# Performance work log

Hardware: AMD Instinct MI355X
Metric: run time of the kernel (lower is better)

## Reference

```python
import jax, jax.numpy as jnp
import numpy as np

EPS = 1e-5

def layer_norm(x, w, b):
    mu = x.mean(-1, keepdims=True)
    var = x.var(-1, keepdims=True)
    return (x - mu) / jnp.sqrt(var + EPS) * w + b

def moe_ffn(y, gW, W1, b1, W2, b2, topk):
    # y: [B,N,d]; W1: [E,d,f]; W2: [E,f,d].  Dense-equivalent of the
    # torch gather/compute/scatter-add dispatch: every expert runs on every
    # token, combined with top-k gate weights (zero for unselected experts).
    gate = jax.nn.softmax(y @ gW, axis=-1)                       # [B,N,E]
    w, sel = jax.lax.top_k(gate, topk)                           # [B,N,k]
    onehot = jax.nn.one_hot(sel, gW.shape[-1], dtype=y.dtype)    # [B,N,k,E]
    comb = jnp.einsum('bnk,bnke->bne', w, onehot)                # combine weights
    hmid = jax.nn.gelu(jnp.einsum('bnd,edf->bnef', y, W1) + b1, approximate=False)
    eo = jnp.einsum('bnef,efd->bned', hmid, W2) + b2             # [B,N,E,d]
    out = jnp.einsum('bne,bned->bnd', comb, eo)
    mask = onehot.sum(2)                                         # [B,N,E] 0/1
    cnt = mask.sum((0, 1))                                       # tokens per expert
    emb = jnp.einsum('bne,bnd->ed', mask, y) / jnp.maximum(cnt, 1.0)[:, None]
    return out, gate, emb

def setup_inputs():
    B, S, N = 8, 512, 1024
    d, H, E, f, L, topk = 512, 8, 8, 8, 2, 2   # d_ff == n_heads (repo quirk)
    key = jax.random.key(0)
    ks = iter(jax.random.split(key, 40))
    g = lambda shape, s=0.02: jax.random.normal(next(ks), shape, jnp.float32) * s
    return dict(
        x=jax.random.normal(next(ks), (B, S, N), jnp.float32),
        revin_w=jnp.ones((N,), jnp.float32) + g((N,), 0.01),
        revin_b=g((N,), 0.01),
        emb_W=g((S, d)), emb_b=g((d,)),
        Wq=g((L, d, d)), bq=g((L, d)),
        Wk=g((L, d, d)), bk=g((L, d)),
        Wv=g((L, d, d)), bv=g((L, d)),
        Wo=g((L, d, d)), bo=g((L, d)),
        ln1_w=jnp.ones((L, d), jnp.float32), ln1_b=jnp.zeros((L, d), jnp.float32),
        ln2_w=jnp.ones((L, d), jnp.float32), ln2_b=jnp.zeros((L, d), jnp.float32),
        gate_W=g((L, d, E)),
        eW1=g((L, E, d, f)), eb1=g((L, E, f)),
        eW2=g((L, E, f, d)), eb2=g((L, E, d)),
        enc_norm_w=jnp.ones((d,), jnp.float32), enc_norm_b=jnp.zeros((d,), jnp.float32),
        head_gate_W=g((d, E)),
        head_W=g((E, d, d)), head_b=g((E, d)),
        topk=topk, n_heads=H,
    )

def reference(x, revin_w, revin_b, emb_W, emb_b, Wq, bq, Wk, bk, Wv, bv, Wo, bo,
              ln1_w, ln1_b, ln2_w, ln2_b, gate_W, eW1, eb1, eW2, eb2,
              enc_norm_w, enc_norm_b, head_gate_W, head_W, head_b, topk, n_heads):
    B, S, N = x.shape
    d = emb_W.shape[1]
    H = n_heads
    dh = d // H
    L = Wq.shape[0]
    # RevIN normalize over time per variable (dropout layers are eval/identity)
    xv = jnp.swapaxes(x, 1, 2)                                   # [B,N,S]
    mean = xv.mean(-1, keepdims=True)
    std = jnp.sqrt(xv.var(-1, keepdims=True) + EPS)
    xn = (xv - mean) / std * revin_w[None, :, None] + revin_b[None, :, None]
    # DataEmbedding_inverted: Linear over the time axis -> variable tokens
    h = xn @ emb_W + emb_b                                       # [B,N,d]
    for l in range(L):
        q = (h @ Wq[l] + bq[l]).reshape(B, N, H, dh)
        k = (h @ Wk[l] + bk[l]).reshape(B, N, H, dh)
        v = (h @ Wv[l] + bv[l]).reshape(B, N, H, dh)
        attn = jax.nn.softmax(jnp.einsum('bnhe,bmhe->bhnm', q, k) / jnp.sqrt(jnp.float32(dh)), axis=-1)
        o = jnp.einsum('bhnm,bmhe->bnhe', attn, v).reshape(B, N, d) @ Wo[l] + bo[l]
        h = layer_norm(h + o, ln1_w[l], ln1_b[l])
        ffn, _gate, _emb = moe_ffn(h, gate_W[l], eW1[l], eb1[l], eW2[l], eb2[l], topk)
        h = layer_norm(h + ffn, ln2_w[l], ln2_b[l])
    h = layer_norm(h, enc_norm_w, enc_norm_b)
    # MoE projection head: experts are Linear(d, d)
    gate = jax.nn.softmax(h @ head_gate_W, axis=-1)
    w, sel = jax.lax.top_k(gate, topk)
    onehot = jax.nn.one_hot(sel, head_gate_W.shape[-1], dtype=h.dtype)
    comb = jnp.einsum('bnk,bnke->bne', w, onehot)
    eo = jnp.einsum('bnd,edf->bnef', h, head_W) + head_b         # [B,N,E,d]
    out = jnp.einsum('bne,bned->bnd', comb, eo)                  # [B,N,d]
    # RevIN denorm applied on [B, d_model, N]
    o2 = jnp.swapaxes(out, 1, 2)
    o2 = (o2 - revin_b[None, None, :]) / (revin_w[None, None, :] + 1e-10)
    o2 = o2 * jnp.swapaxes(std, 1, 2) + jnp.swapaxes(mean, 1, 2)
    return jnp.swapaxes(o2, 1, 2)                                # [B, n_vars, d_model]
```

## Files before the change

kernel.cpp:

```cpp
#include <hip/hip_runtime.h>
#include <math.h>

#define BATCH 8
#define SEQ 512
#define NVAR 1024
#define DM 512
#define NH 8
#define DH 64
#define NE 8
#define NF 8
#define NL 2
#define NTOK (BATCH*NVAR)
#define LN_EPS 1e-5f
#define LSC 2048.0f
#define ILSC (1.0f/2048.0f)

typedef __attribute__((ext_vector_type(8))) _Float16 f16x8;
typedef __attribute__((ext_vector_type(4))) float f32x4;
#define MFMA16 __builtin_amdgcn_mfma_f32_16x16x32_f16

__device__ __forceinline__ void fsplit(float v, _Float16& hi, _Float16& lo) {
    hi = (_Float16)v;
    lo = (_Float16)((v - (float)hi) * LSC);
}
__device__ __forceinline__ float frec(_Float16 hi, _Float16 lo) {
    return (float)hi + (float)lo * ILSC;
}

__device__ __forceinline__ void gload_lds16(const _Float16* g, _Float16* l) {
    __builtin_amdgcn_global_load_lds(
        (const __attribute__((address_space(1))) void*)g,
        (__attribute__((address_space(3))) void*)l, 16, 0, 0);
}

#define DPPROR(v, C) __int_as_float(__builtin_amdgcn_update_dpp(0, __float_as_int(v), (C), 0xF, 0xF, true))
__device__ __forceinline__ float rowmax16(float v) {
    v = fmaxf(v, DPPROR(v, 0x121));
    v = fmaxf(v, DPPROR(v, 0x122));
    v = fmaxf(v, DPPROR(v, 0x124));
    v = fmaxf(v, DPPROR(v, 0x128));
    return v;
}
__device__ __forceinline__ float rowsum16(float v) {
    v += DPPROR(v, 0x121);
    v += DPPROR(v, 0x122);
    v += DPPROR(v, 0x124);
    v += DPPROR(v, 0x128);
    return v;
}

__global__ __launch_bounds__(256) void revin_stats_kernel(
        const float* __restrict__ x, float* __restrict__ mean, float* __restrict__ stdd) {
    int blk = blockIdx.x;
    int b = blk >> 4;
    int n0 = (blk & 15) << 6;
    int t = threadIdx.x;
    int ni = t & 63, sg = t >> 6;
    float s = 0.f, ss = 0.f;
    for (int sidx = sg; sidx < SEQ; sidx += 4) {
        float v = x[((size_t)b*SEQ + sidx)*NVAR + n0 + ni];
        s += v; ss += v*v;
    }
    __shared__ float rs[4][64], rq[4][64];
    rs[sg][ni] = s; rq[sg][ni] = ss;
    __syncthreads();
    if (t < 64) {
        float su = rs[0][t] + rs[1][t] + rs[2][t] + rs[3][t];
        float sq = rq[0][t] + rq[1][t] + rq[2][t] + rq[3][t];
        float m  = su / (float)SEQ;
        float var = sq / (float)SEQ - m*m;
        int n = n0 + t;
        mean[b*NVAR + n] = m;
        stdd[b*NVAR + n] = sqrtf(var + LN_EPS);
    }
}

__global__ __launch_bounds__(256) void revin_norm_kernel(
        const float* __restrict__ x, const float* __restrict__ mean, const float* __restrict__ stdd,
        const float* __restrict__ rw, const float* __restrict__ rb,
        _Float16* __restrict__ xnhi, _Float16* __restrict__ xnlo) {
    __shared__ float tile[32][33];
    int n0 = blockIdx.x << 5, s0 = blockIdx.y << 5, b = blockIdx.z;
    int t = threadIdx.x;
    int j = t & 31, i0 = t >> 5;
    for (int ii = i0; ii < 32; ii += 8)
        tile[ii][j] = x[((size_t)b*SEQ + s0 + ii)*NVAR + n0 + j];
    __syncthreads();
    int si = t & 31, j0 = t >> 5;
    for (int nj = j0; nj < 32; nj += 8) {
        int n = n0 + nj;
        float m = mean[b*NVAR + n], sd = stdd[b*NVAR + n];
        float v = (tile[si][nj] - m) / sd * rw[n] + rb[n];
        _Float16 h_, l_; fsplit(v, h_, l_);
        size_t idx = ((size_t)b*NVAR + n)*SEQ + s0 + si;
        xnhi[idx] = h_; xnlo[idx] = l_;
    }
}

struct WSrcs { const float* p[9]; };
__global__ __launch_bounds__(256) void transpose_w_kernel(
        WSrcs srcs, _Float16* __restrict__ whi, _Float16* __restrict__ wlo) {
    const float* W = srcs.p[blockIdx.z];
    _Float16* oh = whi + (size_t)blockIdx.z * DM * DM;
    _Float16* ol = wlo + (size_t)blockIdx.z * DM * DM;
    __shared__ float tile[64][65];
    int k0 = blockIdx.x << 6, n0 = blockIdx.y << 6;
    int t = threadIdx.x;
    for (int idx = t; idx < 4096; idx += 256) {
        int k = idx >> 6, n = idx & 63;
        tile[k][n] = W[(size_t)(k0 + k)*DM + n0 + n];
    }
    __syncthreads();
    for (int idx = t; idx < 4096; idx += 256) {
        int n = idx >> 6, k = idx & 63;
        _Float16 h_, l_; fsplit(tile[k][n], h_, l_);
        size_t o = (size_t)(n0 + n)*DM + k0 + k;
        oh[o] = h_; ol[o] = l_;
    }
}

__global__ __launch_bounds__(256) void gemm_f16x2_kernel(
        const _Float16* __restrict__ Ahg, const _Float16* __restrict__ Alg,
        const _Float16* __restrict__ Whg, const _Float16* __restrict__ Wlg,
        const float* __restrict__ bias, float* __restrict__ C,
        _Float16* __restrict__ Chi, _Float16* __restrict__ Clo,
        int M, int K, int N) {
    __shared__ _Float16 smem[24576];
    int id = blockIdx.x + (blockIdx.y << 3);
    int rm = ((id & 7) << 6) | (id >> 3);
    int bm = (rm >> 3) << 7, bn = (rm & 7) << 6;
    int t = threadIdx.x;
    int w = t >> 6, lane = t & 63, m16 = lane & 15, quad = lane >> 4;
    int wv = __builtin_amdgcn_readfirstlane(w);
    int lrow = lane >> 2, lcol = (lane & 3) << 3;
    f32x4 a1[2][4] = {}, a2[2][4] = {};

    #define G_STAGE(c, kk) do {                                              \
        _Pragma("unroll")                                                    \
        for (int ch = 0; ch < 2; ++ch) {                                     \
            size_t ga = (size_t)(bm + wv*32 + ch*16 + lrow)*K + (kk) + lcol; \
            gload_lds16(&Ahg[ga], &smem[(c)*4096 + (wv*32 + ch*16)*32]);     \
            gload_lds16(&Alg[ga], &smem[8192 + (c)*4096 + (wv*32 + ch*16)*32]); \
        }                                                                    \
        size_t gb = (size_t)(bn + wv*16 + lrow)*K + (kk) + lcol;             \
        gload_lds16(&Whg[gb], &smem[16384 + (c)*2048 + (wv*16)*32]);         \
        gload_lds16(&Wlg[gb], &smem[20480 + (c)*2048 + (wv*16)*32]);         \
    } while (0)

    G_STAGE(0, 0);
    int cur = 0;
    for (int k0 = 0; k0 < K; k0 += 32, cur ^= 1) {
        __syncthreads();
        if (k0 + 32 < K) G_STAGE(cur ^ 1, k0 + 32);
        const _Float16* AH = &smem[cur*4096];
        const _Float16* AL = &smem[8192 + cur*4096];
        const _Float16* BH = &smem[16384 + cur*2048];
        const _Float16* BL = &smem[20480 + cur*2048];
        f16x8 bh_[4], bl_[4];
#pragma unroll
        for (int nt = 0; nt < 4; ++nt) {
            bh_[nt] = *(const f16x8*)&BH[(nt*16 + m16)*32 + quad*8];
            bl_[nt] = *(const f16x8*)&BL[(nt*16 + m16)*32 + quad*8];
        }
#pragma unroll
        for (int h2 = 0; h2 < 2; ++h2) {
            f16x8 ah = *(const f16x8*)&AH[(w*32 + h2*16 + m16)*32 + quad*8];
            f16x8 al = *(const f16x8*)&AL[(w*32 + h2*16 + m16)*32 + quad*8];
#pragma unroll
            for (int nt = 0; nt < 4; ++nt) {
                a1[h2][nt] = MFMA16(ah, bh_[nt], a1[h2][nt], 0, 0, 0);
                a2[h2][nt] = MFMA16(ah, bl_[nt], a2[h2][nt], 0, 0, 0);
                a2[h2][nt] = MFMA16(al, bh_[nt], a2[h2][nt], 0, 0, 0);
            }
        }
    }
    #undef G_STAGE
#pragma unroll
    for (int h2 = 0; h2 < 2; ++h2)
#pragma unroll
        for (int nt = 0; nt < 4; ++nt) {
            int col = bn + nt*16 + m16;
            float bv = bias[col];
#pragma unroll
            for (int r = 0; r < 4; ++r) {
                size_t row = bm + w*32 + h2*16 + quad*4 + r;
                float v = a1[h2][nt][r] + a2[h2][nt][r]*ILSC + bv;
                if (C) C[row*N + col] = v;
                if (Chi) {
                    _Float16 h_, l_; fsplit(v, h_, l_);
                    Chi[row*N + col] = h_; Clo[row*N + col] = l_;
                }
            }
        }
}

__global__ __launch_bounds__(256) void gemm_f16x2_vt_kernel(
        const _Float16* __restrict__ Ahg, const _Float16* __restrict__ Alg,
        const _Float16* __restrict__ Whg, const _Float16* __restrict__ Wlg,
        const float* __restrict__ bias,
        _Float16* __restrict__ vthi, _Float16* __restrict__ vtlo) {
    __shared__ _Float16 smem[24576];
    int id = blockIdx.x + (blockIdx.y << 3);
    int rm = ((id & 7) << 6) | (id >> 3);
    int bm = (rm >> 3) << 7, bn = (rm & 7) << 6;
    int t = threadIdx.x;
    int w = t >> 6, lane = t & 63, m16 = lane & 15, quad = lane >> 4;
    int wv = __builtin_amdgcn_readfirstlane(w);
    int lrow = lane >> 2, lcol = (lane & 3) << 3;
    f32x4 a1[2][4] = {}, a2[2][4] = {};

    #define G_STAGE(c, kk) do {                                              \
        _Pragma("unroll")                                                    \
        for (int ch = 0; ch < 2; ++ch) {                                     \
            size_t ga = (size_t)(bm + wv*32 + ch*16 + lrow)*DM + (kk) + lcol;\
            gload_lds16(&Ahg[ga], &smem[(c)*4096 + (wv*32 + ch*16)*32]);     \
            gload_lds16(&Alg[ga], &smem[8192 + (c)*4096 + (wv*32 + ch*16)*32]); \
        }                                                                    \
        size_t gb = (size_t)(bn + wv*16 + lrow)*DM + (kk) + lcol;            \
        gload_lds16(&Whg[gb], &smem[16384 + (c)*2048 + (wv*16)*32]);         \
        gload_lds16(&Wlg[gb], &smem[20480 + (c)*2048 + (wv*16)*32]);         \
    } while (0)

    G_STAGE(0, 0);
    int cur = 0;
    for (int k0 = 0; k0 < DM; k0 += 32, cur ^= 1) {
        __syncthreads();
        if (k0 + 32 < DM) G_STAGE(cur ^ 1, k0 + 32);
        const _Float16* AH = &smem[cur*4096];
        const _Float16* AL = &smem[8192 + cur*4096];
        const _Float16* BH = &smem[16384 + cur*2048];
        const _Float16* BL = &smem[20480 + cur*2048];
        f16x8 bh_[4], bl_[4];
#pragma unroll
        for (int nt = 0; nt < 4; ++nt) {
            bh_[nt] = *(const f16x8*)&BH[(nt*16 + m16)*32 + quad*8];
            bl_[nt] = *(const f16x8*)&BL[(nt*16 + m16)*32 + quad*8];
        }
#pragma unroll
        for (int h2 = 0; h2 < 2; ++h2) {
            f16x8 ah = *(const f16x8*)&AH[(w*32 + h2*16 + m16)*32 + quad*8];
            f16x8 al = *(const f16x8*)&AL[(w*32 + h2*16 + m16)*32 + quad*8];
#pragma unroll
            for (int nt = 0; nt < 4; ++nt) {
                a1[h2][nt] = MFMA16(ah, bh_[nt], a1[h2][nt], 0, 0, 0);
                a2[h2][nt] = MFMA16(ah, bl_[nt], a2[h2][nt], 0, 0, 0);
                a2[h2][nt] = MFMA16(al, bh_[nt], a2[h2][nt], 0, 0, 0);
            }
        }
    }
    #undef G_STAGE
    __syncthreads();
    float (*Ct)[65] = (float (*)[65])smem;
#pragma unroll
    for (int h2 = 0; h2 < 2; ++h2)
#pragma unroll
        for (int nt = 0; nt < 4; ++nt) {
            float bv = bias[bn + nt*16 + m16];
#pragma unroll
            for (int r = 0; r < 4; ++r)
                Ct[w*32 + h2*16 + quad*4 + r][nt*16 + m16] = a1[h2][nt][r] + a2[h2][nt][r]*ILSC + bv;
        }
    __syncthreads();
    int b = bm >> 10, tokn0 = bm & 1023, hh = bn >> 6;
    int dh = t >> 2, tg = (t & 3) << 4;
    size_t rowb = ((size_t)(b*8 + hh)*64 + dh)*NVAR + tokn0;
    for (int hb = 0; hb < 2; ++hb) {
        int tl0 = hb*64 + tg;
        unsigned short hbuf[16], lbuf[16];
#pragma unroll
        for (int i = 0; i < 16; ++i) {
            _Float16 h_, l_; fsplit(Ct[tl0 + i][dh], h_, l_);
            hbuf[i] = __builtin_bit_cast(unsigned short, h_);
            lbuf[i] = __builtin_bit_cast(unsigned short, l_);
        }
        uint4 uh0, uh1, ul0, ul1;
        uh0.x = hbuf[0]|(hbuf[1]<<16);  uh0.y = hbuf[2]|(hbuf[3]<<16);
        uh0.z = hbuf[4]|(hbuf[5]<<16);  uh0.w = hbuf[6]|(hbuf[7]<<16);
        uh1.x = hbuf[8]|(hbuf[9]<<16);  uh1.y = hbuf[10]|(hbuf[11]<<16);
        uh1.z = hbuf[12]|(hbuf[13]<<16);uh1.w = hbuf[14]|(hbuf[15]<<16);
        ul0.x = lbuf[0]|(lbuf[1]<<16);  ul0.y = lbuf[2]|(lbuf[3]<<16);
        ul0.z = lbuf[4]|(lbuf[5]<<16);  ul0.w = lbuf[6]|(lbuf[7]<<16);
        ul1.x = lbuf[8]|(lbuf[9]<<16);  ul1.y = lbuf[10]|(lbuf[11]<<16);
        ul1.z = lbuf[12]|(lbuf[13]<<16);ul1.w = lbuf[14]|(lbuf[15]<<16);
        *(uint4*)&vthi[rowb + tl0]     = uh0;
        *(uint4*)&vthi[rowb + tl0 + 8] = uh1;
        *(uint4*)&vtlo[rowb + tl0]     = ul0;
        *(uint4*)&vtlo[rowb + tl0 + 8] = ul1;
    }
}

__global__ __launch_bounds__(256, 4) void attn_f16x2_kernel(
        const _Float16* __restrict__ qh, const _Float16* __restrict__ ql,
        const _Float16* __restrict__ kh, const _Float16* __restrict__ kl,
        const _Float16* __restrict__ vth, const _Float16* __restrict__ vtl,
        _Float16* __restrict__ oh, _Float16* __restrict__ ol) {
    __shared__ _Float16 Kh[64][72], Kl[64][72];
    __shared__ _Float16 Vh[64][72], Vl[64][72];
    int blk = blockIdx.x;
    blk = ((blk & 7) << 7) | (blk >> 3);
    int qt = blk & 15, bh = blk >> 4;
    int b = bh >> 3, hh = bh & 7;
    int q0 = qt << 6;
    int t = threadIdx.x;
    int w = t >> 6, lane = t & 63;
    int m16 = lane & 15, quad = lane >> 4;
    size_t bbase = (size_t)b * NVAR;
    size_t vbase = (size_t)bh * DH * NVAR;

    f16x8 qfh[2], qfl[2];
#pragma unroll
    for (int ks = 0; ks < 2; ++ks) {
        size_t gq = (bbase + q0 + w*16 + m16)*DM + hh*DH + ks*32 + quad*8;
        qfh[ks] = *(const f16x8*)&qh[gq] * (_Float16)0.125f;
        qfl[ks] = *(const f16x8*)&ql[gq] * (_Float16)0.125f;
    }

    float mrow[4] = {-1e30f,-1e30f,-1e30f,-1e30f};
    float lrow[4] = {0.f,0.f,0.f,0.f};
    f32x4 o1[4] = {}, o2[4] = {};

    for (int n0 = 0; n0 < NVAR; n0 += 64) {
        for (int idx = t; idx < 512; idx += 256) {
            int r = idx >> 3, cg = (idx & 7) << 3;
            size_t gk = (bbase + n0 + r)*DM + hh*DH + cg;
            size_t gv = vbase + (size_t)r*NVAR + n0 + cg;
            *(uint4*)&Kh[r][cg] = *(const uint4*)&kh[gk];
            *(uint4*)&Kl[r][cg] = *(const uint4*)&kl[gk];
            *(uint4*)&Vh[r][cg] = *(const uint4*)&vth[gv];
            *(uint4*)&Vl[r][cg] = *(const uint4*)&vtl[gv];
        }
        __syncthreads();

        f32x4 s1[4] = {}, s2[4] = {};
#pragma unroll
        for (int ks = 0; ks < 2; ++ks) {
#pragma unroll
            for (int nt = 0; nt < 4; ++nt) {
                f16x8 bh_ = *(const f16x8*)&Kh[nt*16 + m16][ks*32 + quad*8];
                f16x8 bl_ = *(const f16x8*)&Kl[nt*16 + m16][ks*32 + quad*8];
                s1[nt] = MFMA16(qfh[ks], bh_, s1[nt], 0, 0, 0);
                s2[nt] = MFMA16(qfh[ks], bl_, s2[nt], 0, 0, 0);
                s2[nt] = MFMA16(qfl[ks], bh_, s2[nt], 0, 0, 0);
            }
        }
        __syncthreads();

        float pbuf[4][4];
        float mx[4];
#pragma unroll
        for (int r = 0; r < 4; ++r) {
            float sv0 = fmaf(s2[0][r], ILSC, s1[0][r]);
            float sv1 = fmaf(s2[1][r], ILSC, s1[1][r]);
            float sv2 = fmaf(s2[2][r], ILSC, s1[2][r]);
            float sv3 = fmaf(s2[3][r], ILSC, s1[3][r]);
            pbuf[0][r] = sv0; pbuf[1][r] = sv1; pbuf[2][r] = sv2; pbuf[3][r] = sv3;
            mx[r] = rowmax16(fmaxf(fmaxf(sv0, sv1), fmaxf(sv2, sv3)));
        }
        bool grow = (mx[0] > mrow[0]) | (mx[1] > mrow[1]) |
                    (mx[2] > mrow[2]) | (mx[3] > mrow[3]);
        if (__any(grow)) {
#pragma unroll
            for (int r = 0; r < 4; ++r) {
                float mnew = fmaxf(mrow[r], mx[r]);
                float alpha = __expf(mrow[r] - mnew);
                mrow[r] = mnew;
                lrow[r] *= alpha;
#pragma unroll
                for (int nt = 0; nt < 4; ++nt) { o1[nt][r] *= alpha; o2[nt][r] *= alpha; }
            }
        }
#pragma unroll
        for (int r = 0; r < 4; ++r) {
            float p0 = __expf(pbuf[0][r] - mrow[r]);
            float p1 = __expf(pbuf[1][r] - mrow[r]);
            float p2 = __expf(pbuf[2][r] - mrow[r]);
            float p3 = __expf(pbuf[3][r] - mrow[r]);
            lrow[r] += rowsum16(p0 + p1 + p2 + p3);
            pbuf[0][r] = p0; pbuf[1][r] = p1; pbuf[2][r] = p2; pbuf[3][r] = p3;
        }
#pragma unroll
        for (int nt = 0; nt < 4; ++nt)
#pragma unroll
            for (int r = 0; r < 4; ++r) {
                _Float16 h_, l_; fsplit(pbuf[nt][r], h_, l_);
                Kh[w*16 + quad*4 + r][nt*16 + m16] = h_;
                Kl[w*16 + quad*4 + r][nt*16 + m16] = l_;
            }

#pragma unroll
        for (int ks = 0; ks < 2; ++ks) {
            f16x8 ph = *(const f16x8*)&Kh[w*16 + m16][ks*32 + quad*8];
            f16x8 pl = *(const f16x8*)&Kl[w*16 + m16][ks*32 + quad*8];
#pragma unroll
            for (int nt = 0; nt < 4; ++nt) {
                f16x8 vh_ = *(const f16x8*)&Vh[nt*16 + m16][ks*32 + quad*8];
                f16x8 vl_ = *(const f16x8*)&Vl[nt*16 + m16][ks*32 + quad*8];
                o1[nt] = MFMA16(ph, vh_, o1[nt], 0, 0, 0);
                o2[nt] = MFMA16(ph, vl_, o2[nt], 0, 0, 0);
                o2[nt] = MFMA16(pl, vh_, o2[nt], 0, 0, 0);
            }
        }
        __syncthreads();
    }
#pragma unroll
    for (int r = 0; r < 4; ++r) {
        float inv = 1.0f / lrow[r];
        size_t rowp = (bbase + q0 + w*16 + quad*4 + r)*DM + hh*DH;
#pragma unroll
        for (int nt = 0; nt < 4; ++nt) {
            float ov = fmaf(o2[nt][r], ILSC, o1[nt][r]) * inv;
            _Float16 h_, l_; fsplit(ov, h_, l_);
            oh[rowp + nt*16 + m16] = h_;
            ol[rowp + nt*16 + m16] = l_;
        }
    }
}

__global__ __launch_bounds__(256) void ln_kernel(
        _Float16* __restrict__ hhi, _Float16* __restrict__ hlo,
        const float* __restrict__ res,
        const float* __restrict__ w, const float* __restrict__ b) {
    int rowi = blockIdx.x, t = threadIdx.x;
    size_t base = (size_t)rowi * DM;
    int c = t << 1;
    unsigned int uh = *(const unsigned int*)&hhi[base + c];
    unsigned int ul = *(const unsigned int*)&hlo[base + c];
    _Float16 h0 = __builtin_bit_cast(_Float16, (unsigned short)(uh & 0xFFFF));
    _Float16 h1 = __builtin_bit_cast(_Float16, (unsigned short)(uh >> 16));
    _Float16 l0 = __builtin_bit_cast(_Float16, (unsigned short)(ul & 0xFFFF));
    _Float16 l1 = __builtin_bit_cast(_Float16, (unsigned short)(ul >> 16));
    float v0 = frec(h0, l0);
    float v1 = frec(h1, l1);
    if (res) { float2 rv = *(const float2*)&res[base + c]; v0 += rv.x; v1 += rv.y; }
    float s = v0 + v1, q = v0*v0 + v1*v1;
#pragma unroll
    for (int off = 1; off < 64; off <<= 1) {
        s += __shfl_xor(s, off);
        q += __shfl_xor(q, off);
    }
    __shared__ float sred[4], qred[4];
    int wid = t >> 6, lane = t & 63;
    if (lane == 0) { sred[wid] = s; qred[wid] = q; }
    __syncthreads();
    s = sred[0] + sred[1] + sred[2] + sred[3];
    q = qred[0] + qred[1] + qred[2] + qred[3];
    float m = s / (float)DM;
    float var = q / (float)DM - m*m;
    float inv = 1.0f / sqrtf(var + LN_EPS);
    float2 wv = *(const float2*)&w[c];
    float2 bv = *(const float2*)&b[c];
    float y0 = (v0 - m)*inv * wv.x + bv.x;
    float y1 = (v1 - m)*inv * wv.y + bv.y;
    _Float16 h0o, l0o, h1o, l1o;
    fsplit(y0, h0o, l0o); fsplit(y1, h1o, l1o);
    *(unsigned int*)&hhi[base + c] =
        (unsigned int)__builtin_bit_cast(unsigned short, h0o) |
        ((unsigned int)__builtin_bit_cast(unsigned short, h1o) << 16);
    *(unsigned int*)&hlo[base + c] =
        (unsigned int)__builtin_bit_cast(unsigned short, l0o) |
        ((unsigned int)__builtin_bit_cast(unsigned short, l1o) << 16);
}

__device__ __forceinline__ float gelu_exact(float xv) {
    return 0.5f * xv * (1.0f + erff(xv * 0.70710678118654752f));
}

__global__ __launch_bounds__(256) void moe_kernel(
        const _Float16* __restrict__ hhi, const _Float16* __restrict__ hlo,
        float* __restrict__ out,
        const float* __restrict__ gW, const float* __restrict__ W1, const float* __restrict__ b1,
        const float* __restrict__ W2, const float* __restrict__ b2) {
    int tok = blockIdx.x, t = threadIdx.x;
    __shared__ float hs[DM];
    __shared__ float red[32][8];
    __shared__ float glog[8];
    __shared__ float hmid[8];
    __shared__ float wsel[2];
    __shared__ int   esel[2];
    size_t base = (size_t)tok * DM;
    hs[t] = frec(hhi[base + t], hlo[base + t]);
    hs[t + 256] = frec(hhi[base + t + 256], hlo[base + t + 256]);
    __syncthreads();
    int e = t & 7, i0 = t >> 3;
    {
        float a = 0.f;
        for (int i = i0; i < DM; i += 32) a += hs[i] * gW[i*NE + e];
        red[i0][e] = a;
    }
    __syncthreads();
    if (t < 8) { float sv = 0.f; for (int i = 0; i < 32; ++i) sv += red[i][t]; glog[t] = sv; }
    __syncthreads();
    if (t == 0) {
        float m0 = -1e30f, m1 = -1e30f; int s0i = 0, s1i = 0;
        for (int ei = 0; ei < 8; ++ei) {
            float vv = glog[ei];
            if (vv > m0) { m1 = m0; s1i = s0i; m0 = vv; s0i = ei; }
            else if (vv > m1) { m1 = vv; s1i = ei; }
        }
        float Z = 0.f;
        for (int ei = 0; ei < 8; ++ei) Z += expf(glog[ei] - m0);
        wsel[0] = 1.0f / Z;
        wsel[1] = expf(m1 - m0) / Z;
        esel[0] = s0i; esel[1] = s1i;
    }
    __syncthreads();
    float o0 = 0.f, o1 = 0.f;
    for (int ks = 0; ks < 2; ++ks) {
        int ee = esel[ks]; float wk = wsel[ks];
        int f = t & 7;
        float a = 0.f;
        for (int i = i0; i < DM; i += 32) a += hs[i] * W1[((size_t)ee*DM + i)*NF + f];
        red[i0][f] = a;
        __syncthreads();
        if (t < 8) {
            float sv = b1[ee*NF + t];
            for (int i = 0; i < 32; ++i) sv += red[i][t];
            hmid[t] = gelu_exact(sv);
        }
        __syncthreads();
        float s0v = b2[ee*DM + t], s1v = b2[ee*DM + t + 256];
#pragma unroll
        for (int i = 0; i < NF; ++i) {
            float hm = hmid[i];
            const float* wp = W2 + ((size_t)ee*NF + i)*DM;
            s0v += hm * wp[t]; s1v += hm * wp[t + 256];
        }
        o0 += wk * s0v; o1 += wk * s1v;
        __syncthreads();
    }
    out[base + t] = o0; out[base + t + 256] = o1;
}

__global__ __launch_bounds__(64) void head_init_kernel(int* __restrict__ cnt) {
    if (threadIdx.x < NE) cnt[threadIdx.x] = 0;
}

__global__ __launch_bounds__(256) void head_gate_kernel(
        const _Float16* __restrict__ hhi, const _Float16* __restrict__ hlo,
        const float* __restrict__ gW,
        int* __restrict__ sel, float2* __restrict__ wpair) {
    int tok = blockIdx.x, t = threadIdx.x;
    __shared__ float hs[DM];
    __shared__ float red[32][8];
    __shared__ float glog[8];
    size_t base = (size_t)tok * DM;
    hs[t] = frec(hhi[base + t], hlo[base + t]);
    hs[t + 256] = frec(hhi[base + t + 256], hlo[base + t + 256]);
    __syncthreads();
    int e = t & 7, i0 = t >> 3;
    float a = 0.f;
    for (int i = i0; i < DM; i += 32) a += hs[i] * gW[i*NE + e];
    red[i0][e] = a;
    __syncthreads();
    if (t < 8) { float sv = 0.f; for (int i = 0; i < 32; ++i) sv += red[i][t]; glog[t] = sv; }
    __syncthreads();
    if (t == 0) {
        float m0 = -1e30f, m1 = -1e30f; int s0i = 0, s1i = 0;
        for (int ei = 0; ei < 8; ++ei) {
            float vv = glog[ei];
            if (vv > m0) { m1 = m0; s1i = s0i; m0 = vv; s0i = ei; }
            else if (vv > m1) { m1 = vv; s1i = ei; }
        }
        float Z = 0.f;
        for (int ei = 0; ei < 8; ++ei) Z += __expf(glog[ei] - m0);
        float2 wv;
        wv.x = 1.0f / Z;
        wv.y = __expf(m1 - m0) / Z;
        sel[tok] = s0i | (s1i << 3);
        wpair[tok] = wv;
    }
}

__global__ __launch_bounds__(64) void head_bucket_kernel(
        const int* __restrict__ sel, const float2* __restrict__ wpair,
        int* __restrict__ cnt, int* __restrict__ idxlist, float* __restrict__ wlist,
        int* __restrict__ pos0, int* __restrict__ pos1) {
    int lane = threadIdx.x;
    int tok = blockIdx.x*64 + lane;
    int s = sel[tok];
    int s0 = s & 7, s1 = (s >> 3) & 7;
    float2 wv = wpair[tok];
    unsigned long long lmask = (lane == 63) ? 0x7FFFFFFFFFFFFFFFull
                                            : ((1ull << lane) - 1ull);
#pragma unroll
    for (int e = 0; e < NE; ++e) {
        unsigned long long m0 = __ballot(s0 == e);
        unsigned long long m1 = __ballot(s1 == e);
        int tot = __popcll(m0) + __popcll(m1);
        int basep = 0;
        if (lane == 0 && tot > 0) basep = atomicAdd(&cnt[e], tot);
        basep = __shfl(basep, 0);
        if (s0 == e) {
            int p = basep + __popcll(m0 & lmask);
            idxlist[e*NTOK + p] = tok; wlist[e*NTOK + p] = wv.x;
            pos0[tok] = (e << 16) | p;
        }
        if (s1 == e) {
            int p = basep + __popcll(m0) + __popcll(m1 & lmask);
            idxlist[e*NTOK + p] = tok; wlist[e*NTOK + p] = wv.y;
            pos1[tok] = (e << 16) | p;
        }
    }
}

__global__ __launch_bounds__(64) void head_prefix_kernel(int* __restrict__ cnt) {
    if (threadIdx.x == 0) {
        int run = 0, trun = 0;
        for (int e = 0; e < NE; ++e) {
            cnt[8 + e]  = run;  run  += cnt[e];
            cnt[16 + e] = trun; trun += (cnt[e] + 63) >> 6;
        }
        cnt[24] = trun;
    }
}

__global__ __launch_bounds__(256) void head_gemm_f16x2_kernel(
        const _Float16* __restrict__ hhi, const _Float16* __restrict__ hlo,
        const _Float16* __restrict__ hwhi, const _Float16* __restrict__ hwlo,
        const float* __restrict__ Hb,
        const int* __restrict__ cnt, const int* __restrict__ idxlist,
        const float* __restrict__ wlist, float* __restrict__ slotf) {
    int item = blockIdx.x;
    int total = cnt[24];
    if (item >= 2*total) return;
    int bn   = (item & 1) << 8;
    int tile = item >> 1;
    int e = 0;
#pragma unroll
    for (int ei = 1; ei < NE; ++ei) if (tile >= cnt[16 + ei]) e = ei;
    int m0 = (tile - cnt[16 + e]) << 6;
    int cnt_e = cnt[e];
    int rv = cnt_e - m0; if (rv > 64) rv = 64;
    int pref_e = cnt[8 + e];
    int t = threadIdx.x;
    int w = t >> 6, lane = t & 63, m16 = lane & 15, quad = lane >> 4;

    __shared__ _Float16 sAh[64][40], sAl[64][40];
    __shared__ _Float16 sBh[256][40], sBl[256][40];
    __shared__ int   idxs[64];
    __shared__ float ws[64];
    if (t < 64) {
        if (t < rv) { idxs[t] = idxlist[e*NTOK + m0 + t]; ws[t] = wlist[e*NTOK + m0 + t]; }
        else        { idxs[t] = idxlist[e*NTOK + m0];     ws[t] = 0.f; }
    }
    __syncthreads();

    const _Float16* Wh = hwhi + (size_t)e*DM*DM;
    const _Float16* Wl = hwlo + (size_t)e*DM*DM;
    int ra = t >> 2, ca = (t & 3) << 3;
    f32x4 a1[4][4] = {}, a2[4][4] = {};
    for (int k0 = 0; k0 < DM; k0 += 32) {
        size_t ga = (size_t)idxs[ra]*DM + k0 + ca;
        *(uint4*)&sAh[ra][ca] = *(const uint4*)&hhi[ga];
        *(uint4*)&sAl[ra][ca] = *(const uint4*)&hlo[ga];
#pragma unroll
        for (int p = 0; p < 4; ++p) {
            int rb = p*64 + ra;
            size_t gb = (size_t)(bn + rb)*DM + k0 + ca;
            *(uint4*)&sBh[rb][ca] = *(const uint4*)&Wh[gb];
            *(uint4*)&sBl[rb][ca] = *(const uint4*)&Wl[gb];
        }
        __syncthreads();
        f16x8 ah[4], al[4];
#pragma unroll
        for (int mt = 0; mt < 4; ++mt) {
            ah[mt] = *(const f16x8*)&sAh[mt*16 + m16][quad*8];
            al[mt] = *(const f16x8*)&sAl[mt*16 + m16][quad*8];
        }
#pragma unroll
        for (int nt = 0; nt < 4; ++nt) {
            f16x8 bh_ = *(const f16x8*)&sBh[w*64 + nt*16 + m16][quad*8];
            f16x8 bl_ = *(const f16x8*)&sBl[w*64 + nt*16 + m16][quad*8];
#pragma unroll
            for (int mt = 0; mt < 4; ++mt) {
                a1[mt][nt] = MFMA16(ah[mt], bh_, a1[mt][nt], 0, 0, 0);
                a2[mt][nt] = MFMA16(ah[mt], bl_, a2[mt][nt], 0, 0, 0);
                a2[mt][nt] = MFMA16(al[mt], bh_, a2[mt][nt], 0, 0, 0);
            }
        }
        __syncthreads();
    }
#pragma unroll
    for (int mt = 0; mt < 4; ++mt)
#pragma unroll
        for (int r = 0; r < 4; ++r) {
            int rloc = mt*16 + quad*4 + r;
            if (rloc < rv) {
                float wk = ws[rloc];
                size_t srow = (size_t)(pref_e + m0 + rloc)*DM;
#pragma unroll
                for (int nt = 0; nt < 4; ++nt) {
                    int gcol = bn + w*64 + nt*16 + m16;
                    float v = a1[mt][nt][r] + a2[mt][nt][r]*ILSC + Hb[e*DM + gcol];
                    slotf[srow + gcol] = wk * v;
                }
            }
        }
}

__global__ __launch_bounds__(256) void head_combine_kernel(
        const float* __restrict__ slotf,
        const int* __restrict__ pos0, const int* __restrict__ pos1,
        const int* __restrict__ cnt,
        const float* __restrict__ rw, const float* __restrict__ rb,
        const float* __restrict__ mean, const float* __restrict__ stdd,
        float* __restrict__ out) {
    int tok = blockIdx.x, t = threadIdx.x;
    int n = tok & (NVAR - 1);
    int e0enc = pos0[tok], e1enc = pos1[tok];
    size_t s0 = (size_t)(cnt[8 + (e0enc >> 16)] + (e0enc & 0xFFFF)) * DM;
    size_t s1 = (size_t)(cnt[8 + (e1enc >> 16)] + (e1enc & 0xFFFF)) * DM;
    size_t base = (size_t)tok * DM;
    float mn = mean[tok], sd = stdd[tok];
    float rwv = rw[n] + 1e-10f, rbv = rb[n];
    float o0 = slotf[s0 + t] + slotf[s1 + t];
    float o1 = slotf[s0 + t + 256] + slotf[s1 + t + 256];
    out[base + t]       = (o0 - rbv) / rwv * sd + mn;
    out[base + t + 256] = (o1 - rbv) / rwv * sd + mn;
}

extern "C" void kernel_launch(void* const* d_in, const int* in_sizes, int n_in,
                              void* d_out, int out_size, void* d_ws, size_t ws_size,
                              hipStream_t stream) {
    const float* x       = (const float*)d_in[0];
    const float* revin_w = (const float*)d_in[1];
    const float* revin_b = (const float*)d_in[2];
    const float* emb_W   = (const float*)d_in[3];
    const float* emb_b   = (const float*)d_in[4];
    const float* Wq      = (const float*)d_in[5];
    const float* bq      = (const float*)d_in[6];
    const float* Wk      = (const float*)d_in[7];
    const float* bk      = (const float*)d_in[8];
    const float* Wv      = (const float*)d_in[9];
    const float* bv      = (const float*)d_in[10];
    const float* Wo      = (const float*)d_in[11];
    const float* bo      = (const float*)d_in[12];
    const float* ln1_w   = (const float*)d_in[13];
    const float* ln1_b   = (const float*)d_in[14];
    const float* ln2_w   = (const float*)d_in[15];
    const float* ln2_b   = (const float*)d_in[16];
    const float* gate_W  = (const float*)d_in[17];
    const float* eW1     = (const float*)d_in[18];
    const float* eb1     = (const float*)d_in[19];
    const float* eW2     = (const float*)d_in[20];
    const float* eb2     = (const float*)d_in[21];
    const float* enc_w   = (const float*)d_in[22];
    const float* enc_b   = (const float*)d_in[23];
    const float* hgW     = (const float*)d_in[24];
    const float* hW      = (const float*)d_in[25];
    const float* hb      = (const float*)d_in[26];
    float* out = (float*)d_out;

    const size_t TOKD = (size_t)NTOK * DM;
    float* ws   = (float*)d_ws;
    float* mean = ws;
    float* stdd = ws + 8192;
    _Float16* hhi  = (_Float16*)(ws + 16384);
    _Float16* hlo  = hhi + TOKD;
    _Float16* qhi  = hlo + TOKD;
    _Float16* qlo  = qhi + TOKD;
    _Float16* khi  = qlo + TOKD;
    _Float16* klo  = khi + TOKD;
    _Float16* vthi = klo + TOKD;
    _Float16* vtlo = vthi + TOKD;
    _Float16* whi  = vtlo + TOKD;
    _Float16* wlo  = whi + (size_t)9*DM*DM;
    int*   cnt     = (int*)(wlo + (size_t)9*DM*DM);
    int*   idxlist = cnt + 32;
    float* wlist   = (float*)(idxlist + NE*NTOK);
    int*   sel     = (int*)(wlist + NE*NTOK);
    float2* wpair  = (float2*)(sel + NTOK);
    int*   pos0    = (int*)(wpair + NTOK);
    int*   pos1    = pos0 + NTOK;
    float* proj    = (float*)khi;
    float* slotf   = (float*)qhi;

    dim3 blk(256);
    dim3 ggemm(DM/64, NTOK/128);

    revin_stats_kernel<<<dim3(BATCH*16), blk, 0, stream>>>(x, mean, stdd);
    revin_norm_kernel<<<dim3(NVAR/32, SEQ/32, BATCH), blk, 0, stream>>>(
        x, mean, stdd, revin_w, revin_b, qhi, qlo);

    WSrcs srcs;
    srcs.p[0] = emb_W;
    for (int l = 0; l < NL; ++l) {
        srcs.p[1 + l*4 + 0] = Wq + (size_t)l*DM*DM;
        srcs.p[1 + l*4 + 1] = Wk + (size_t)l*DM*DM;
        srcs.p[1 + l*4 + 2] = Wv + (size_t)l*DM*DM;
        srcs.p[1 + l*4 + 3] = Wo + (size_t)l*DM*DM;
    }
    transpose_w_kernel<<<dim3(8, 8, 9), blk, 0, stream>>>(srcs, whi, wlo);

    gemm_f16x2_kernel<<<ggemm, blk, 0, stream>>>(
        qhi, qlo, whi, wlo, emb_b, nullptr, hhi, hlo, NTOK, SEQ, DM);

    for (int l = 0; l < NL; ++l) {
        size_t oq = (size_t)(1 + l*4 + 0)*DM*DM;
        size_t ok = (size_t)(1 + l*4 + 1)*DM*DM;
        size_t ov = (size_t)(1 + l*4 + 2)*DM*DM;
        size_t oo = (size_t)(1 + l*4 + 3)*DM*DM;
        gemm_f16x2_kernel<<<ggemm, blk, 0, stream>>>(
            hhi, hlo, whi + oq, wlo + oq, bq + l*DM, nullptr, qhi, qlo, NTOK, DM, DM);
        gemm_f16x2_kernel<<<ggemm, blk, 0, stream>>>(
            hhi, hlo, whi + ok, wlo + ok, bk + l*DM, nullptr, khi, klo, NTOK, DM, DM);
        gemm_f16x2_vt_kernel<<<ggemm, blk, 0, stream>>>(
            hhi, hlo, whi + ov, wlo + ov, bv + l*DM, vthi, vtlo);
        attn_f16x2_kernel<<<dim3(64*16), blk, 0, stream>>>(
            qhi, qlo, khi, klo, vthi, vtlo, qhi, qlo);
        gemm_f16x2_kernel<<<ggemm, blk, 0, stream>>>(
            qhi, qlo, whi + oo, wlo + oo, bo + l*DM, proj, nullptr, nullptr, NTOK, DM, DM);
        ln_kernel<<<dim3(NTOK), blk, 0, stream>>>(hhi, hlo, proj, ln1_w + l*DM, ln1_b + l*DM);
        moe_kernel<<<dim3(NTOK), blk, 0, stream>>>(
            hhi, hlo, proj, gate_W + (size_t)l*DM*NE,
            eW1 + (size_t)l*NE*DM*NF, eb1 + (size_t)l*NE*NF,
            eW2 + (size_t)l*NE*NF*DM, eb2 + (size_t)l*NE*DM);
        ln_kernel<<<dim3(NTOK), blk, 0, stream>>>(hhi, hlo, proj, ln2_w + l*DM, ln2_b + l*DM);
    }

    ln_kernel<<<dim3(NTOK), blk, 0, stream>>>(hhi, hlo, nullptr, enc_w, enc_b);

    WSrcs hsrcs;
    for (int e = 0; e < NE; ++e) hsrcs.p[e] = hW + (size_t)e*DM*DM;
    hsrcs.p[8] = hW;
    transpose_w_kernel<<<dim3(8, 8, 8), blk, 0, stream>>>(hsrcs, vthi, vtlo);

    head_init_kernel<<<dim3(1), dim3(64), 0, stream>>>(cnt);
    head_gate_kernel<<<dim3(NTOK), blk, 0, stream>>>(hhi, hlo, hgW, sel, wpair);
    head_bucket_kernel<<<dim3(NTOK/64), dim3(64), 0, stream>>>(
        sel, wpair, cnt, idxlist, wlist, pos0, pos1);
    head_prefix_kernel<<<dim3(1), dim3(64), 0, stream>>>(cnt);
    head_gemm_f16x2_kernel<<<dim3(576), blk, 0, stream>>>(
        hhi, hlo, vthi, vtlo, hb, cnt, idxlist, wlist, slotf);
    head_combine_kernel<<<dim3(NTOK), blk, 0, stream>>>(
        slotf, pos0, pos1, cnt, revin_w, revin_b, mean, stdd, out);
}
```

Baseline: 826.0 us.

## Fuse Q/K projections into one GEMM and fold layer norms into MoE and head gate

Merges the Q and K projection GEMMs into one launch that treats the two weight matrices as a single N=1024 output, relying on Wq and Wk being stored back to back in the transposed weight buffer. Fuses the post-MoE residual add and LayerNorm into the MoE kernel, so the fp32 proj round trip and a separate LN launch go away. Also fuses the final encoder LayerNorm into the head gate kernel. These cut launches and global memory traffic. The cost is a larger per-block epilogue and a dependence on the weight buffer layout.

```diff
diff --git a/kernel.cpp b/kernel.cpp
--- a/kernel.cpp
+++ b/kernel.cpp
@@ -190,6 +190,82 @@
                     _Float16 h_, l_; fsplit(v, h_, l_);
                     Chi[row*N + col] = h_; Clo[row*N + col] = l_;
                 }
+            }
+        }
+}
+
+__global__ __launch_bounds__(256) void gemm_qk_kernel(
+        const _Float16* __restrict__ Ahg, const _Float16* __restrict__ Alg,
+        const _Float16* __restrict__ Whg, const _Float16* __restrict__ Wlg,
+        const float* __restrict__ biasQ, const float* __restrict__ biasK,
+        _Float16* __restrict__ Qhi, _Float16* __restrict__ Qlo,
+        _Float16* __restrict__ KKhi, _Float16* __restrict__ KKlo) {
+    __shared__ _Float16 smem[24576];
+    int id = blockIdx.x;
+    int rm = ((id & 7) << 7) | (id >> 3);
+    int bm = (rm >> 4) << 7, bn = (rm & 15) << 6;
+    int t = threadIdx.x;
+    int w = t >> 6, lane = t & 63, m16 = lane & 15, quad = lane >> 4;
+    int wv = __builtin_amdgcn_readfirstlane(w);
+    int lrow = lane >> 2, lcol = (lane & 3) << 3;
+    f32x4 a1[2][4] = {}, a2[2][4] = {};
+
+    #define G_STAGE(c, kk) do {                                              \
+        _Pragma("unroll")                                                    \
+        for (int ch = 0; ch < 2; ++ch) {                                     \
+            size_t ga = (size_t)(bm + wv*32 + ch*16 + lrow)*DM + (kk) + lcol;\
+            gload_lds16(&Ahg[ga], &smem[(c)*4096 + (wv*32 + ch*16)*32]);     \
+            gload_lds16(&Alg[ga], &smem[8192 + (c)*4096 + (wv*32 + ch*16)*32]); \
+        }                                                                    \
+        size_t gb = (size_t)(bn + wv*16 + lrow)*DM + (kk) + lcol;            \
+        gload_lds16(&Whg[gb], &smem[16384 + (c)*2048 + (wv*16)*32]);         \
+        gload_lds16(&Wlg[gb], &smem[20480 + (c)*2048 + (wv*16)*32]);         \
+    } while (0)
+
+    G_STAGE(0, 0);
+    int cur = 0;
+    for (int k0 = 0; k0 < DM; k0 += 32, cur ^= 1) {
+        __syncthreads();
+        if (k0 + 32 < DM) G_STAGE(cur ^ 1, k0 + 32);
+        const _Float16* AH = &smem[cur*4096];
+        const _Float16* AL = &smem[8192 + cur*4096];
+        const _Float16* BH = &smem[16384 + cur*2048];
+        const _Float16* BL = &smem[20480 + cur*2048];
+        f16x8 bh_[4], bl_[4];
+#pragma unroll
+        for (int nt = 0; nt < 4; ++nt) {
+            bh_[nt] = *(const f16x8*)&BH[(nt*16 + m16)*32 + quad*8];
+            bl_[nt] = *(const f16x8*)&BL[(nt*16 + m16)*32 + quad*8];
+        }
+#pragma unroll
+        for (int h2 = 0; h2 < 2; ++h2) {
+            f16x8 ah = *(const f16x8*)&AH[(w*32 + h2*16 + m16)*32 + quad*8];
+            f16x8 al = *(const f16x8*)&AL[(w*32 + h2*16 + m16)*32 + quad*8];
+#pragma unroll
+            for (int nt = 0; nt < 4; ++nt) {
+                a1[h2][nt] = MFMA16(ah, bh_[nt], a1[h2][nt], 0, 0, 0);
+                a2[h2][nt] = MFMA16(ah, bl_[nt], a2[h2][nt], 0, 0, 0);
+                a2[h2][nt] = MFMA16(al, bh_[nt], a2[h2][nt], 0, 0, 0);
+            }
+        }
+    }
+    #undef G_STAGE
+    const float* bias = (bn < 512) ? biasQ : biasK;
+    _Float16* Ohi = (bn < 512) ? Qhi : KKhi;
+    _Float16* Olo = (bn < 512) ? Qlo : KKlo;
+    int cb = (bn < 512) ? bn : bn - 512;
+#pragma unroll
+    for (int h2 = 0; h2 < 2; ++h2)
+#pragma unroll
+        for (int nt = 0; nt < 4; ++nt) {
+            int col = cb + nt*16 + m16;
+            float bv = bias[col];
+#pragma unroll
+            for (int r = 0; r < 4; ++r) {
+                size_t row = bm + w*32 + h2*16 + quad*4 + r;
+                float v = a1[h2][nt][r] + a2[h2][nt][r]*ILSC + bv;
+                _Float16 h_, l_; fsplit(v, h_, l_);
+                Ohi[row*DM + col] = h_; Olo[row*DM + col] = l_;
             }
         }
 }
@@ -465,11 +541,11 @@
     return 0.5f * xv * (1.0f + erff(xv * 0.70710678118654752f));
 }
 
-__global__ __launch_bounds__(256) void moe_kernel(
-        const _Float16* __restrict__ hhi, const _Float16* __restrict__ hlo,
-        float* __restrict__ out,
+__global__ __launch_bounds__(256) void moe_ln_kernel(
+        _Float16* __restrict__ hhi, _Float16* __restrict__ hlo,
         const float* __restrict__ gW, const float* __restrict__ W1, const float* __restrict__ b1,
-        const float* __restrict__ W2, const float* __restrict__ b2) {
+        const float* __restrict__ W2, const float* __restrict__ b2,
+        const float* __restrict__ lw, const float* __restrict__ lb) {
     int tok = blockIdx.x, t = threadIdx.x;
     __shared__ float hs[DM];
     __shared__ float red[32][8];
@@ -477,9 +553,16 @@
     __shared__ float hmid[8];
     __shared__ float wsel[2];
     __shared__ int   esel[2];
+    __shared__ float sred[4], qred[4];
     size_t base = (size_t)tok * DM;
-    hs[t] = frec(hhi[base + t], hlo[base + t]);
-    hs[t + 256] = frec(hhi[base + t + 256], hlo[base + t + 256]);
+    int c = t << 1;
+    unsigned int uh = *(const unsigned int*)&hhi[base + c];
+    unsigned int ul = *(const unsigned int*)&hlo[base + c];
+    float hv0 = frec(__builtin_bit_cast(_Float16, (unsigned short)(uh & 0xFFFF)),
+                     __builtin_bit_cast(_Float16, (unsigned short)(ul & 0xFFFF)));
+    float hv1 = frec(__builtin_bit_cast(_Float16, (unsigned short)(uh >> 16)),
+                     __builtin_bit_cast(_Float16, (unsigned short)(ul >> 16)));
+    hs[c] = hv0; hs[c + 1] = hv1;
     __syncthreads();
     int e = t & 7, i0 = t >> 3;
     {
@@ -518,34 +601,91 @@
             hmid[t] = gelu_exact(sv);
         }
         __syncthreads();
-        float s0v = b2[ee*DM + t], s1v = b2[ee*DM + t + 256];
+        float2 b2v = *(const float2*)&b2[ee*DM + c];
+        float s0v = b2v.x, s1v = b2v.y;
 #pragma unroll
         for (int i = 0; i < NF; ++i) {
             float hm = hmid[i];
-            const float* wp = W2 + ((size_t)ee*NF + i)*DM;
-            s0v += hm * wp[t]; s1v += hm * wp[t + 256];
+            float2 wpv = *(const float2*)&W2[((size_t)ee*NF + i)*DM + c];
+            s0v += hm * wpv.x; s1v += hm * wpv.y;
         }
         o0 += wk * s0v; o1 += wk * s1v;
         __syncthreads();
     }
-    out[base + t] = o0; out[base + t + 256] = o1;
-}
-
-__global__ __launch_bounds__(64) void head_init_kernel(int* __restrict__ cnt) {
-    if (threadIdx.x < NE) cnt[threadIdx.x] = 0;
-}
-
-__global__ __launch_bounds__(256) void head_gate_kernel(
-        const _Float16* __restrict__ hhi, const _Float16* __restrict__ hlo,
+    float v0 = hv0 + o0, v1 = hv1 + o1;
+    float s = v0 + v1, q = v0*v0 + v1*v1;
+#pragma unroll
+    for (int off = 1; off < 64; off <<= 1) {
+        s += __shfl_xor(s, off);
+        q += __shfl_xor(q, off);
+    }
+    int wid = t >> 6, lane = t & 63;
+    if (lane == 0) { sred[wid] = s; qred[wid] = q; }
+    __syncthreads();
+    s = sred[0] + sred[1] + sred[2] + sred[3];
+    q = qred[0] + qred[1] + qred[2] + qred[3];
+    float m = s / (float)DM;
+    float var = q / (float)DM - m*m;
+    float inv = 1.0f / sqrtf(var + LN_EPS);
+    float2 wv = *(const float2*)&lw[c];
+    float2 bv = *(const float2*)&lb[c];
+    float y0 = (v0 - m)*inv * wv.x + bv.x;
+    float y1 = (v1 - m)*inv * wv.y + bv.y;
+    _Float16 h0o, l0o, h1o, l1o;
+    fsplit(y0, h0o, l0o); fsplit(y1, h1o, l1o);
+    *(unsigned int*)&hhi[base + c] =
+        (unsigned int)__builtin_bit_cast(unsigned short, h0o) |
+        ((unsigned int)__builtin_bit_cast(unsigned short, h1o) << 16);
+    *(unsigned int*)&hlo[base + c] =
+        (unsigned int)__builtin_bit_cast(unsigned short, l0o) |
+        ((unsigned int)__builtin_bit_cast(unsigned short, l1o) << 16);
+}
+
+__global__ __launch_bounds__(256) void encln_gate_kernel(
+        _Float16* __restrict__ hhi, _Float16* __restrict__ hlo,
+        const float* __restrict__ lw, const float* __restrict__ lb,
         const float* __restrict__ gW,
         int* __restrict__ sel, float2* __restrict__ wpair) {
     int tok = blockIdx.x, t = threadIdx.x;
     __shared__ float hs[DM];
     __shared__ float red[32][8];
     __shared__ float glog[8];
+    __shared__ float sred[4], qred[4];
     size_t base = (size_t)tok * DM;
-    hs[t] = frec(hhi[base + t], hlo[base + t]);
-    hs[t + 256] = frec(hhi[base + t + 256], hlo[base + t + 256]);
+    int c = t << 1;
+    unsigned int uh = *(const unsigned int*)&hhi[base + c];
+    unsigned int ul = *(const unsigned int*)&hlo[base + c];
+    float v0 = frec(__builtin_bit_cast(_Float16, (unsigned short)(uh & 0xFFFF)),
+                    __builtin_bit_cast(_Float16, (unsigned short)(ul & 0xFFFF)));
+    float v1 = frec(__builtin_bit_cast(_Float16, (unsigned short)(uh >> 16)),
+                    __builtin_bit_cast(_Float16, (unsigned short)(ul >> 16)));
+    float s = v0 + v1, q = v0*v0 + v1*v1;
+#pragma unroll
+    for (int off = 1; off < 64; off <<= 1) {
+        s += __shfl_xor(s, off);
+        q += __shfl_xor(q, off);
+    }
+    int wid = t >> 6, lane = t & 63;
+    if (lane == 0) { sred[wid] = s; qred[wid] = q; }
+    __syncthreads();
+    s = sred[0] + sred[1] + sred[2] + sred[3];
+    q = qred[0] + qred[1] + qred[2] + qred[3];
+    float m = s / (float)DM;
+    float var = q / (float)DM - m*m;
+    float inv = 1.0f / sqrtf(var + LN_EPS);
+    float2 wv = *(const float2*)&lw[c];
+    float2 bv = *(const float2*)&lb[c];
+    float y0 = (v0 - m)*inv * wv.x + bv.x;
+    float y1 = (v1 - m)*inv * wv.y + bv.y;
+    _Float16 h0o, l0o, h1o, l1o;
+    fsplit(y0, h0o, l0o); fsplit(y1, h1o, l1o);
+    *(unsigned int*)&hhi[base + c] =
+        (unsigned int)__builtin_bit_cast(unsigned short, h0o) |
+        ((unsigned int)__builtin_bit_cast(unsigned short, h1o) << 16);
+    *(unsigned int*)&hlo[base + c] =
+        (unsigned int)__builtin_bit_cast(unsigned short, l0o) |
+        ((unsigned int)__builtin_bit_cast(unsigned short, l1o) << 16);
+    hs[c] = y0; hs[c + 1] = y1;
     __syncthreads();
     int e = t & 7, i0 = t >> 3;
     float a = 0.f;
@@ -563,12 +703,16 @@
         }
         float Z = 0.f;
         for (int ei = 0; ei < 8; ++ei) Z += __expf(glog[ei] - m0);
-        float2 wv;
-        wv.x = 1.0f / Z;
-        wv.y = __expf(m1 - m0) / Z;
+        float2 wvv;
+        wvv.x = 1.0f / Z;
+        wvv.y = __expf(m1 - m0) / Z;
         sel[tok] = s0i | (s1i << 3);
-        wpair[tok] = wv;
-    }
+        wpair[tok] = wvv;
+    }
+}
+
+__global__ __launch_bounds__(64) void head_init_kernel(int* __restrict__ cnt) {
+    if (threadIdx.x < NE) cnt[threadIdx.x] = 0;
 }
 
 __global__ __launch_bounds__(64) void head_bucket_kernel(
@@ -797,13 +941,11 @@
 
     for (int l = 0; l < NL; ++l) {
         size_t oq = (size_t)(1 + l*4 + 0)*DM*DM;
-        size_t ok = (size_t)(1 + l*4 + 1)*DM*DM;
         size_t ov = (size_t)(1 + l*4 + 2)*DM*DM;
         size_t oo = (size_t)(1 + l*4 + 3)*DM*DM;
-        gemm_f16x2_kernel<<<ggemm, blk, 0, stream>>>(
-            hhi, hlo, whi + oq, wlo + oq, bq + l*DM, nullptr, qhi, qlo, NTOK, DM, DM);
-        gemm_f16x2_kernel<<<ggemm, blk, 0, stream>>>(
-            hhi, hlo, whi + ok, wlo + ok, bk + l*DM, nullptr, khi, klo, NTOK, DM, DM);
+        gemm_qk_kernel<<<dim3(1024), blk, 0, stream>>>(
+            hhi, hlo, whi + oq, wlo + oq, bq + l*DM, bk + l*DM,
+            qhi, qlo, khi, klo);
         gemm_f16x2_vt_kernel<<<ggemm, blk, 0, stream>>>(
             hhi, hlo, whi + ov, wlo + ov, bv + l*DM, vthi, vtlo);
         attn_f16x2_kernel<<<dim3(64*16), blk, 0, stream>>>(
@@ -811,14 +953,12 @@
         gemm_f16x2_kernel<<<ggemm, blk, 0, stream>>>(
             qhi, qlo, whi + oo, wlo + oo, bo + l*DM, proj, nullptr, nullptr, NTOK, DM, DM);
         ln_kernel<<<dim3(NTOK), blk, 0, stream>>>(hhi, hlo, proj, ln1_w + l*DM, ln1_b + l*DM);
-        moe_kernel<<<dim3(NTOK), blk, 0, stream>>>(
-            hhi, hlo, proj, gate_W + (size_t)l*DM*NE,
+        moe_ln_kernel<<<dim3(NTOK), blk, 0, stream>>>(
+            hhi, hlo, gate_W + (size_t)l*DM*NE,
             eW1 + (size_t)l*NE*DM*NF, eb1 + (size_t)l*NE*NF,
-            eW2 + (size_t)l*NE*NF*DM, eb2 + (size_t)l*NE*DM);
-        ln_kernel<<<dim3(NTOK), blk, 0, stream>>>(hhi, hlo, proj, ln2_w + l*DM, ln2_b + l*DM);
-    }
-
-    ln_kernel<<<dim3(NTOK), blk, 0, stream>>>(hhi, hlo, nullptr, enc_w, enc_b);
+            eW2 + (size_t)l*NE*NF*DM, eb2 + (size_t)l*NE*DM,
+            ln2_w + l*DM, ln2_b + l*DM);
+    }
 
     WSrcs hsrcs;
     for (int e = 0; e < NE; ++e) hsrcs.p[e] = hW + (size_t)e*DM*DM;
@@ -826,7 +966,8 @@
     transpose_w_kernel<<<dim3(8, 8, 8), blk, 0, stream>>>(hsrcs, vthi, vtlo);
 
     head_init_kernel<<<dim3(1), dim3(64), 0, stream>>>(cnt);
-    head_gate_kernel<<<dim3(NTOK), blk, 0, stream>>>(hhi, hlo, hgW, sel, wpair);
+    encln_gate_kernel<<<dim3(NTOK), blk, 0, stream>>>(
+        hhi, hlo, enc_w, enc_b, hgW, sel, wpair);
     head_bucket_kernel<<<dim3(NTOK/64), dim3(64), 0, stream>>>(
         sel, wpair, cnt, idxlist, wlist, pos0, pos1);
     head_prefix_kernel<<<dim3(1), dim3(64), 0, stream>>>(cnt);
```

After: 812.3 us. No clear change (-1.7%).
